# Optimization experiments

Hardware: AMD Instinct MI355X
Metric: run time of the kernel (lower is better)

## Reference

```python
import jax, jax.numpy as jnp
import numpy as np

N_NODES = 50000
EPS = 1e-5


def sage_conv_max(x, src, dst, W_l, b_l, W_r):
    # PyG SAGEConv(aggr='max'): out = lin_l(max_j x_j) + lin_r(x_i)
    msg = x[src]                                   # [E, d] gather
    agg = jnp.full((x.shape[0], x.shape[1]), -jnp.inf, dtype=x.dtype)
    agg = agg.at[dst].max(msg)                     # scatter-max over edges
    agg = jnp.where(jnp.isneginf(agg), 0.0, agg)   # isolated nodes -> 0 (PyG convention)
    return agg @ W_l.T + b_l + x @ W_r.T


def batch_norm(x, gamma, beta):
    mean = jnp.mean(x, axis=0)
    var = jnp.var(x, axis=0)
    return (x - mean) * jax.lax.rsqrt(var + EPS) * gamma + beta


def setup_inputs() -> dict:
    key = jax.random.key(0)
    ks = jax.random.split(key, 10)
    d_in, d_h, d_out = 128, 128, 32
    s = lambda fan: 1.0 / np.sqrt(fan)
    return {
        "x": jax.random.normal(ks[0], (N_NODES, d_in), dtype=jnp.float32),
        "edge_index": jax.random.randint(ks[1], (2, 800000), 0, N_NODES, dtype=jnp.int32),
        "W_l1": jax.random.uniform(ks[2], (d_h, d_in), jnp.float32, -s(d_in), s(d_in)),
        "b_l1": jnp.zeros((d_h,), jnp.float32),
        "W_r1": jax.random.uniform(ks[3], (d_h, d_in), jnp.float32, -s(d_in), s(d_in)),
        "gamma1": jnp.ones((d_h,), jnp.float32),
        "beta1": jnp.zeros((d_h,), jnp.float32),
        "W_l2": jax.random.uniform(ks[4], (d_out, d_h), jnp.float32, -s(d_h), s(d_h)),
        "b_l2": jnp.zeros((d_out,), jnp.float32),
        "W_r2": jax.random.uniform(ks[5], (d_out, d_h), jnp.float32, -s(d_h), s(d_h)),
    }


def reference(x, edge_index, W_l1, b_l1, W_r1, gamma1, beta1, W_l2, b_l2, W_r2):
    src, dst = edge_index[0], edge_index[1]
    h = sage_conv_max(x, src, dst, W_l1, b_l1, W_r1)
    h = batch_norm(h, gamma1, beta1)
    h = jax.nn.relu(h)
    # dropout is identity at inference
    return sage_conv_max(h, src, dst, W_l2, b_l2, W_r2)
```

## Files before the change

### kernel.cpp

```cpp
#include <hip/hip_runtime.h>
#include <math.h>
#include <float.h>

#define N_NODES 50000
#define N_EDGES 800000
#define NB 392
#define EB 2048
#define NBUCK 196
#define BSH 8
#define CAP 36
#define SEGC 4864
#define CELLS_PER_BUCKET (NB * CAP)

typedef __attribute__((ext_vector_type(8))) short bf16x8;
typedef __attribute__((ext_vector_type(4))) float f32x4;

static __device__ __forceinline__ unsigned short f2bf(float f) {
  unsigned int u = __float_as_uint(f);
  u = (u + 0x7fff + ((u >> 16) & 1)) >> 16;
  return (unsigned short)u;
}

__global__ __launch_bounds__(256) void setup_kernel(
    const int* __restrict__ src, const int* __restrict__ dst,
    unsigned int* __restrict__ pairs, int* __restrict__ counts,
    const float* __restrict__ x, const float* __restrict__ Wl1,
    const float* __restrict__ Wr1, const float* __restrict__ Wl2,
    const float* __restrict__ Wr2, unsigned int* __restrict__ x_bf,
    unsigned short* __restrict__ Wcat1, unsigned short* __restrict__ Wcat2,
    float* __restrict__ gsums) {
  const int b = blockIdx.x, tid = threadIdx.x;
  if (b < NB) {
    __shared__ int cur[NBUCK];
    if (tid < NBUCK) cur[tid] = 0;
    __syncthreads();
#pragma unroll
    for (int it = 0; it < EB / 256; ++it) {
      int e = b * EB + it * 256 + tid;
      if (e < N_EDGES) {
        int d = dst[e];
        int bk = d >> BSH;
        int p = atomicAdd(&cur[bk], 1);
        if (p < CAP)
          pairs[(size_t)(bk * NB + b) * CAP + p] =
              (unsigned)src[e] | ((unsigned)(d & 255) << 16);
      }
    }
    __syncthreads();
    if (tid < NBUCK) {
      int c = cur[tid];
      counts[tid * NB + b] = c > CAP ? CAP : c;
    }
  } else if (b < NB + 6250) {
    int i = (b - NB) * 256 + tid;
    float4 v = ((const float4*)x)[i];
    uint2 o;
    o.x = (unsigned int)f2bf(v.x) | ((unsigned int)f2bf(v.y) << 16);
    o.y = (unsigned int)f2bf(v.z) | ((unsigned int)f2bf(v.w) << 16);
    ((uint2*)x_bf)[i] = o;
  } else if (b < NB + 6410) {
    int i = (b - NB - 6250) * 256 + tid;
    if (i < 32768) {
      int n = i >> 8, k = i & 255;
      float w = (k < 128) ? Wl1[n * 128 + k] : Wr1[n * 128 + (k - 128)];
      Wcat1[i] = f2bf(w);
    } else if (i < 40960) {
      int j = i - 32768;
      int n = j >> 8, k = j & 255;
      float w = (k < 128) ? Wl2[n * 128 + k] : Wr2[n * 128 + (k - 128)];
      Wcat2[j] = f2bf(w);
    }
  } else {
#pragma unroll
    for (int i = 0; i < 8; ++i) gsums[i * 256 + tid] = 0.f;
  }
}

__global__ __launch_bounds__(1024) void bucket_sort(const unsigned int* __restrict__ pairs,
                                                    const int* __restrict__ counts,
                                                    unsigned int* __restrict__ rowinfo,
                                                    int* __restrict__ elist) {
  __shared__ int hist[256], cpos[256], cnt[NB];
  __shared__ int wsum[4];
  const int b = blockIdx.x, tid = threadIdx.x;
  const size_t s0 = (size_t)b * CELLS_PER_BUCKET;
  if (tid < 256) hist[tid] = 0;
  if (tid < NB) cnt[tid] = counts[b * NB + tid];
  __syncthreads();
  for (int p = tid; p < CELLS_PER_BUCKET; p += 1024) {
    int c = p / CAP, s = p - c * CAP;
    if (s < cnt[c]) {
      unsigned int pr = pairs[s0 + p];
      atomicAdd(&hist[(pr >> 16) & 255], 1);
    }
  }
  __syncthreads();
  int incl = 0, h = 0;
  if (tid < 256) {
    const int l = tid & 63;
    h = hist[tid];
    incl = h;
#pragma unroll
    for (int off = 1; off < 64; off <<= 1) {
      int t = __shfl_up(incl, off, 64);
      if (l >= off) incl += t;
    }
    if (l == 63) wsum[tid >> 6] = incl;
  }
  __syncthreads();
  if (tid < 64) {
    int v = (tid < 4) ? wsum[tid] : 0;
#pragma unroll
    for (int off = 1; off < 4; off <<= 1) {
      int t = __shfl_up(v, off, 64);
      if (tid >= off) v += t;
    }
    if (tid < 4) wsum[tid] = v;
  }
  __syncthreads();
  if (tid < 256) {
    const int w = tid >> 6;
    int tot = incl + ((w > 0) ? wsum[w - 1] : 0);
    int excl = tot - h;
    cpos[tid] = excl;
    int node = (b << BSH) + tid;
    if (node < N_NODES)
      rowinfo[node] = (unsigned)(b * SEGC + excl) | ((unsigned)h << 20);
  }
  __syncthreads();
  for (int p = tid; p < CELLS_PER_BUCKET; p += 1024) {
    int c = p / CAP, s = p - c * CAP;
    if (s < cnt[c]) {
      unsigned int pr = pairs[s0 + p];
      int loc = atomicAdd(&cpos[(pr >> 16) & 255], 1);
      elist[b * SEGC + loc] = (int)(pr & 0xffffu);
    }
  }
}

template <bool BN>
__global__ __launch_bounds__(256) void agg_max_bf16(const uint4* __restrict__ feat4,
                                                    const unsigned int* __restrict__ rowinfo,
                                                    const int* __restrict__ elist,
                                                    const float* __restrict__ gsums,
                                                    const float* __restrict__ gamma,
                                                    const float* __restrict__ beta,
                                                    uint4* __restrict__ out4) {
  __shared__ float s_scale[128], s_shift[128];
  if (BN) {
    int t = threadIdx.x;
    if (t < 128) {
      float sm = 0.f, sq = 0.f;
#pragma unroll
      for (int r = 0; r < 8; ++r) {
        sm += gsums[r * 256 + t];
        sq += gsums[r * 256 + 128 + t];
      }
      const float inv = 1.f / (float)N_NODES;
      float mean = sm * inv;
      float var = sq * inv - mean * mean;
      float sc = gamma[t] * rsqrtf(var + 1e-5f);
      s_scale[t] = sc;
      s_shift[t] = beta[t] - mean * sc;
    }
    __syncthreads();
  }

  int node = blockIdx.x * 4 + (threadIdx.x >> 6);
  int lane = threadIdx.x & 63;
  int eslot = lane >> 4;
  int fq = lane & 15;
  unsigned int info = rowinfo[node];
  int e0 = (int)(info & 0xFFFFFu);
  int deg = (int)(info >> 20);
  int e1 = e0 + deg;
  float m[8];
#pragma unroll
  for (int j = 0; j < 8; ++j) m[j] = -FLT_MAX;

  if (deg > 0) {
    const int last = e1 - 1;
    for (int base = e0; base < e1; base += 16) {
      int idx[4];
#pragma unroll
      for (int q = 0; q < 4; ++q) {
        int e = base + q * 4 + eslot;
        if (e > last) e = last;
        idx[q] = elist[e];
      }
      uint4 v[4];
#pragma unroll
      for (int q = 0; q < 4; ++q) v[q] = feat4[(size_t)idx[q] * 16 + fq];
#pragma unroll
      for (int q = 0; q < 4; ++q) {
        const unsigned int* pv = (const unsigned int*)&v[q];
#pragma unroll
        for (int c = 0; c < 4; ++c) {
          m[2 * c]     = fmaxf(m[2 * c],     __uint_as_float(pv[c] << 16));
          m[2 * c + 1] = fmaxf(m[2 * c + 1], __uint_as_float(pv[c] & 0xffff0000u));
        }
      }
    }
  }

#pragma unroll
  for (int j = 0; j < 8; ++j) {
    m[j] = fmaxf(m[j], __shfl_xor(m[j], 16, 64));
    m[j] = fmaxf(m[j], __shfl_xor(m[j], 32, 64));
  }
  if (eslot == 0) {
    if (deg == 0) {
#pragma unroll
      for (int j = 0; j < 8; ++j) m[j] = 0.f;
    } else if (BN) {
#pragma unroll
      for (int j = 0; j < 8; ++j) {
        int col = fq * 8 + j;
        m[j] = fmaxf(m[j] * s_scale[col] + s_shift[col], 0.f);
      }
    }
    uint4 o;
    o.x = (unsigned)f2bf(m[0]) | ((unsigned)f2bf(m[1]) << 16);
    o.y = (unsigned)f2bf(m[2]) | ((unsigned)f2bf(m[3]) << 16);
    o.z = (unsigned)f2bf(m[4]) | ((unsigned)f2bf(m[5]) << 16);
    o.w = (unsigned)f2bf(m[6]) | ((unsigned)f2bf(m[7]) << 16);
    out4[(size_t)node * 16 + fq] = o;
  }
}

template <int NT, bool BF16OUT, bool STATS, bool BNIN>
__global__ __launch_bounds__(256) void gemm_mfma(
    const unsigned short* __restrict__ Aa, const unsigned short* __restrict__ Ab,
    const unsigned short* __restrict__ Wcat, const float* __restrict__ bias,
    unsigned short* __restrict__ outb, float* __restrict__ outf,
    float* __restrict__ gsums, const float* __restrict__ gamma,
    const float* __restrict__ beta, int N) {
  __shared__ float s_sum[128], s_sq[128];
  __shared__ float s_scale[128], s_shift[128];
  const int tid = threadIdx.x;
  const int rowBase = blockIdx.x * 64;

  if (STATS && tid < 128) { s_sum[tid] = 0.f; s_sq[tid] = 0.f; }
  if (BNIN && tid < 128) {
    float sm = 0.f, sq = 0.f;
#pragma unroll
    for (int r = 0; r < 8; ++r) {
      sm += gsums[r * 256 + tid];
      sq += gsums[r * 256 + 128 + tid];
    }
    const float inv = 1.f / (float)N_NODES;
    float mean = sm * inv;
    float var = sq * inv - mean * mean;
    float sc = gamma[tid] * rsqrtf(var + 1e-5f);
    s_scale[tid] = sc;
    s_shift[tid] = beta[tid] - mean * sc;
  }
  __syncthreads();

  const int wv = tid >> 6;
  const int lane = tid & 63;
  const int ln15 = lane & 15;
  const int quad = lane >> 4;
  const int mrow = rowBase + wv * 16;
  int r0 = mrow + ln15;
  if (r0 >= N) r0 = N - 1;

  f32x4 acc[NT] = {};

#pragma unroll
  for (int ks = 0; ks < 8; ++ks) {
    const int off = ks * 32 + quad * 8;
    bf16x8 a;
    if (ks < 4) {
      a = *(const bf16x8*)(Aa + (size_t)r0 * 128 + off);
    } else {
      const int kb = off - 128;
      a = *(const bf16x8*)(Ab + (size_t)r0 * 128 + kb);
      if (BNIN) {
        unsigned int* p = (unsigned int*)&a;
#pragma unroll
        for (int c = 0; c < 4; ++c) {
          int k = kb + 2 * c;
          float lo = __uint_as_float(p[c] << 16);
          float hi = __uint_as_float(p[c] & 0xffff0000u);
          lo = fmaxf(lo * s_scale[k] + s_shift[k], 0.f);
          hi = fmaxf(hi * s_scale[k + 1] + s_shift[k + 1], 0.f);
          p[c] = (unsigned)f2bf(lo) | ((unsigned)f2bf(hi) << 16);
        }
      }
    }
#pragma unroll
    for (int nt = 0; nt < NT; ++nt) {
      bf16x8 b = *(const bf16x8*)(Wcat + (size_t)(nt * 16 + ln15) * 256 + off);
      acc[nt] = __builtin_amdgcn_mfma_f32_16x16x32_bf16(a, b, acc[nt], 0, 0, 0);
    }
  }

  const int ldo = NT * 16;
#pragma unroll
  for (int nt = 0; nt < NT; ++nt) {
    int col = nt * 16 + ln15;
    float bv = bias[col];
    float psum = 0.f, psq = 0.f;
#pragma unroll
    for (int i = 0; i < 4; ++i) {
      int r = mrow + quad * 4 + i;
      if (r < N) {
        float val = acc[nt][i] + bv;
        if (STATS) { psum += val; psq += val * val; }
        if (BF16OUT)
          outb[(size_t)r * ldo + col] = f2bf(val);
        else
          outf[(size_t)r * ldo + col] = val;
      }
    }
    if (STATS) {
      atomicAdd(&s_sum[col], psum);
      atomicAdd(&s_sq[col], psq);
    }
  }
  if (STATS) {
    __syncthreads();
    if (tid < 128) {
      int rep = blockIdx.x & 7;
      atomicAdd(&gsums[rep * 256 + tid], s_sum[tid]);
      atomicAdd(&gsums[rep * 256 + 128 + tid], s_sq[tid]);
    }
  }
}

extern "C" void kernel_launch(void* const* d_in, const int* in_sizes, int n_in,
                              void* d_out, int out_size, void* d_ws, size_t ws_size,
                              hipStream_t stream) {
  (void)in_sizes; (void)n_in; (void)out_size; (void)ws_size;
  const float* x     = (const float*)d_in[0];
  const int*   eidx  = (const int*)d_in[1];
  const float* W_l1  = (const float*)d_in[2];
  const float* b_l1  = (const float*)d_in[3];
  const float* W_r1  = (const float*)d_in[4];
  const float* gamma = (const float*)d_in[5];
  const float* beta  = (const float*)d_in[6];
  const float* W_l2  = (const float*)d_in[7];
  const float* b_l2  = (const float*)d_in[8];
  const float* W_r2  = (const float*)d_in[9];
  const int* srcp = eidx;
  const int* dstp = eidx + N_EDGES;
  float* out = (float*)d_out;

  int* wsi = (int*)d_ws;
  float* gsums   = (float*)wsi;
  unsigned int* rowinfo = (unsigned int*)(wsi + 2048);
  int*   counts  = wsi + 52224;
  int*   elist   = wsi + 129056;
  unsigned int* pairs   = (unsigned int*)(wsi + 1082400);
  unsigned int* x_bf    = (unsigned int*)(wsi + 3848352);
  unsigned int* agg_bf  = (unsigned int*)(wsi + 7048352);
  unsigned int* h_bf    = (unsigned int*)(wsi + 10248352);
  unsigned short* Wcat1 = (unsigned short*)(wsi + 13448352);
  unsigned short* Wcat2 = (unsigned short*)(wsi + 13464736);

  setup_kernel<<<dim3(NB + 6410 + 1), 256, 0, stream>>>(
      srcp, dstp, pairs, counts, x, W_l1, W_r1, W_l2, W_r2, x_bf, Wcat1, Wcat2, gsums);

  bucket_sort<<<dim3(NBUCK), 1024, 0, stream>>>(pairs, counts, rowinfo, elist);

  agg_max_bf16<false><<<dim3(N_NODES / 4), 256, 0, stream>>>(
      (const uint4*)x_bf, rowinfo, elist, nullptr, nullptr, nullptr, (uint4*)agg_bf);
  gemm_mfma<8, true, true, false><<<dim3(784), 256, 0, stream>>>(
      (const unsigned short*)agg_bf, (const unsigned short*)x_bf, Wcat1, b_l1,
      (unsigned short*)h_bf, nullptr, gsums, nullptr, nullptr, N_NODES);

  agg_max_bf16<true><<<dim3(N_NODES / 4), 256, 0, stream>>>(
      (const uint4*)h_bf, rowinfo, elist, gsums, gamma, beta, (uint4*)agg_bf);
  gemm_mfma<2, false, false, true><<<dim3(784), 256, 0, stream>>>(
      (const unsigned short*)agg_bf, (const unsigned short*)h_bf, Wcat2, b_l2,
      nullptr, out, gsums, gamma, beta, N_NODES);
}
```

Baseline: 233.9 us.

## Hold weight fragments in registers and reassign waves to column or row tiles

```diff
diff --git a/kernel.cpp b/kernel.cpp
--- a/kernel.cpp
+++ b/kernel.cpp
@@ -228,8 +228,8 @@
   }
 }
 
-template <int NT, bool BF16OUT, bool STATS, bool BNIN>
-__global__ __launch_bounds__(256) void gemm_mfma(
+template <bool COLSPLIT, int LDO, bool BF16OUT, bool STATS, bool BNIN>
+__global__ __launch_bounds__(256) void gemm_breg(
     const unsigned short* __restrict__ Aa, const unsigned short* __restrict__ Ab,
     const unsigned short* __restrict__ Wcat, const float* __restrict__ bias,
     unsigned short* __restrict__ outb, float* __restrict__ outf,
@@ -238,7 +238,6 @@
   __shared__ float s_sum[128], s_sq[128];
   __shared__ float s_scale[128], s_shift[128];
   const int tid = threadIdx.x;
-  const int rowBase = blockIdx.x * 64;
 
   if (STATS && tid < 128) { s_sum[tid] = 0.f; s_sq[tid] = 0.f; }
   if (BNIN && tid < 128) {
@@ -255,71 +254,87 @@
     s_scale[tid] = sc;
     s_shift[tid] = beta[tid] - mean * sc;
   }
-  __syncthreads();
+  if (STATS || BNIN) __syncthreads();
 
   const int wv = tid >> 6;
   const int lane = tid & 63;
   const int ln15 = lane & 15;
   const int quad = lane >> 4;
-  const int mrow = rowBase + wv * 16;
-  int r0 = mrow + ln15;
-  if (r0 >= N) r0 = N - 1;
-
-  f32x4 acc[NT] = {};
-
+  const int ct0 = COLSPLIT ? wv * 2 : 0;
+  const int rowBase = COLSPLIT ? blockIdx.x * 64
+                               : blockIdx.x * 256 + wv * 64;
+
+  bf16x8 breg[8][2];
 #pragma unroll
   for (int ks = 0; ks < 8; ++ks) {
     const int off = ks * 32 + quad * 8;
-    bf16x8 a;
-    if (ks < 4) {
-      a = *(const bf16x8*)(Aa + (size_t)r0 * 128 + off);
-    } else {
-      const int kb = off - 128;
-      a = *(const bf16x8*)(Ab + (size_t)r0 * 128 + kb);
-      if (BNIN) {
-        unsigned int* p = (unsigned int*)&a;
-#pragma unroll
-        for (int c = 0; c < 4; ++c) {
-          int k = kb + 2 * c;
-          float lo = __uint_as_float(p[c] << 16);
-          float hi = __uint_as_float(p[c] & 0xffff0000u);
-          lo = fmaxf(lo * s_scale[k] + s_shift[k], 0.f);
-          hi = fmaxf(hi * s_scale[k + 1] + s_shift[k + 1], 0.f);
-          p[c] = (unsigned)f2bf(lo) | ((unsigned)f2bf(hi) << 16);
+#pragma unroll
+    for (int j = 0; j < 2; ++j)
+      breg[ks][j] = *(const bf16x8*)(Wcat + (size_t)((ct0 + j) * 16 + ln15) * 256 + off);
+  }
+
+  float psum[2] = {0.f, 0.f}, psq[2] = {0.f, 0.f};
+
+#pragma unroll
+  for (int s = 0; s < 4; ++s) {
+    const int mrow = rowBase + s * 16;
+    int r0 = mrow + ln15;
+    if (r0 >= N) r0 = N - 1;
+    bf16x8 a[8];
+#pragma unroll
+    for (int ks = 0; ks < 8; ++ks) {
+      const int off = ks * 32 + quad * 8;
+      if (ks < 4) {
+        a[ks] = *(const bf16x8*)(Aa + (size_t)r0 * 128 + off);
+      } else {
+        const int kb = off - 128;
+        a[ks] = *(const bf16x8*)(Ab + (size_t)r0 * 128 + kb);
+        if (BNIN) {
+          unsigned int* p = (unsigned int*)&a[ks];
+#pragma unroll
+          for (int c = 0; c < 4; ++c) {
+            int k = kb + 2 * c;
+            float lo = __uint_as_float(p[c] << 16);
+            float hi = __uint_as_float(p[c] & 0xffff0000u);
+            lo = fmaxf(lo * s_scale[k] + s_shift[k], 0.f);
+            hi = fmaxf(hi * s_scale[k + 1] + s_shift[k + 1], 0.f);
+            p[c] = (unsigned)f2bf(lo) | ((unsigned)f2bf(hi) << 16);
+          }
         }
       }
     }
-#pragma unroll
-    for (int nt = 0; nt < NT; ++nt) {
-      bf16x8 b = *(const bf16x8*)(Wcat + (size_t)(nt * 16 + ln15) * 256 + off);
-      acc[nt] = __builtin_amdgcn_mfma_f32_16x16x32_bf16(a, b, acc[nt], 0, 0, 0);
-    }
-  }
-
-  const int ldo = NT * 16;
-#pragma unroll
-  for (int nt = 0; nt < NT; ++nt) {
-    int col = nt * 16 + ln15;
-    float bv = bias[col];
-    float psum = 0.f, psq = 0.f;
-#pragma unroll
-    for (int i = 0; i < 4; ++i) {
-      int r = mrow + quad * 4 + i;
-      if (r < N) {
-        float val = acc[nt][i] + bv;
-        if (STATS) { psum += val; psq += val * val; }
-        if (BF16OUT)
-          outb[(size_t)r * ldo + col] = f2bf(val);
-        else
-          outf[(size_t)r * ldo + col] = val;
-      }
-    }
-    if (STATS) {
-      atomicAdd(&s_sum[col], psum);
-      atomicAdd(&s_sq[col], psq);
-    }
-  }
+    f32x4 acc[2] = {};
+#pragma unroll
+    for (int ks = 0; ks < 8; ++ks)
+#pragma unroll
+      for (int j = 0; j < 2; ++j)
+        acc[j] = __builtin_amdgcn_mfma_f32_16x16x32_bf16(a[ks], breg[ks][j], acc[j], 0, 0, 0);
+#pragma unroll
+    for (int j = 0; j < 2; ++j) {
+      int col = (ct0 + j) * 16 + ln15;
+      float bv = bias[col];
+#pragma unroll
+      for (int i = 0; i < 4; ++i) {
+        int r = mrow + quad * 4 + i;
+        if (r < N) {
+          float val = acc[j][i] + bv;
+          if (STATS) { psum[j] += val; psq[j] += val * val; }
+          if (BF16OUT)
+            outb[(size_t)r * LDO + col] = f2bf(val);
+          else
+            outf[(size_t)r * LDO + col] = val;
+        }
+      }
+    }
+  }
+
   if (STATS) {
+#pragma unroll
+    for (int j = 0; j < 2; ++j) {
+      int col = (ct0 + j) * 16 + ln15;
+      atomicAdd(&s_sum[col], psum[j]);
+      atomicAdd(&s_sq[col], psq[j]);
+    }
     __syncthreads();
     if (tid < 128) {
       int rep = blockIdx.x & 7;
@@ -366,13 +381,13 @@
 
   agg_max_bf16<false><<<dim3(N_NODES / 4), 256, 0, stream>>>(
       (const uint4*)x_bf, rowinfo, elist, nullptr, nullptr, nullptr, (uint4*)agg_bf);
-  gemm_mfma<8, true, true, false><<<dim3(784), 256, 0, stream>>>(
+  gemm_breg<true, 128, true, true, false><<<dim3(784), 256, 0, stream>>>(
       (const unsigned short*)agg_bf, (const unsigned short*)x_bf, Wcat1, b_l1,
       (unsigned short*)h_bf, nullptr, gsums, nullptr, nullptr, N_NODES);
 
   agg_max_bf16<true><<<dim3(N_NODES / 4), 256, 0, stream>>>(
       (const uint4*)h_bf, rowinfo, elist, gsums, gamma, beta, (uint4*)agg_bf);
-  gemm_mfma<2, false, false, true><<<dim3(784), 256, 0, stream>>>(
+  gemm_breg<false, 32, false, false, true><<<dim3(196), 256, 0, stream>>>(
       (const unsigned short*)agg_bf, (const unsigned short*)h_bf, Wcat2, b_l2,
       nullptr, out, gsums, gamma, beta, N_NODES);
 }
```

After: 205.7 us. 12.1% less time.
